# Kernel tuning notes

Hardware: AMD Instinct MI355X
Metric: run time of the kernel (lower is better)

Reference implementation:

```python
import jax, jax.numpy as jnp
import numpy as np

EMB = 300; H = 150; DEC = 300
VU = 50000; VQ = 30000; VS = 5000
N_COLS = 64; COL_LEN = 6; N_TURNS = 6; IN_LEN = 128; GEN_LEN = 64
MAX_KEEP = 5


def _lstm_cell(x, h, c, Wih, Whh, b):
    z = x @ Wih.T + h @ Whh.T + b
    i, f, g, o = jnp.split(z, 4)
    c = jax.nn.sigmoid(f) * c + jax.nn.sigmoid(i) * jnp.tanh(g)
    h = jax.nn.sigmoid(o) * jnp.tanh(c)
    return h, c


def _run_lstm(xs, Wih, Whh, b):
    hsz = Whh.shape[-1]
    z = jnp.zeros((hsz,), xs.dtype)
    def step(carry, x):
        h, c = _lstm_cell(x, carry[0], carry[1], Wih, Whh, b)
        return (h, c), h
    (h, c), ys = jax.lax.scan(step, (z, z), xs)
    return ys, h, c


def _bilstm(xs, Wih, Whh, b):
    # Wih: [2, 4H, in], Whh: [2, 4H, H], b: [2, 4H]
    yf, hf, cf = _run_lstm(xs, Wih[0], Whh[0], b[0])
    yb, hb, cb = _run_lstm(xs[::-1], Wih[1], Whh[1], b[1])
    return jnp.concatenate([yf, yb[::-1]], -1), jnp.concatenate([hf, hb], -1), jnp.concatenate([cf, cb], -1)


def _attention(q, keys, Wq, Wk, v):
    # Bahdanau: v^T tanh(Wq q + Wk k); context = softmax-weighted sum of keys
    s = jnp.tanh(q @ Wq + keys @ Wk) @ v
    return jax.nn.softmax(s) @ keys


def _forward(utter_emb, query_emb, schema_tok_emb, enc_Wih, enc_Whh, enc_b,
             attn_Wq, attn_Wk, attn_v, dec_Wih0, dec_Whh0, dec_b0,
             dec_Wih1, dec_Whh1, dec_b1, transform_W, sql_W, sql_b, col_W,
             schema_tokens, input_seqs, output_gt):
    attn = lambda k_i, q, keys: _attention(q, keys, attn_Wq[k_i], attn_Wk[k_i], attn_v[k_i])
    # --- schema column encoding: BiLSTM over each column's name tokens ---
    col_tok = schema_tok_emb[schema_tokens]                       # [C, L, EMB]
    _, h, _ = jax.vmap(lambda xs: _bilstm(xs, enc_Wih[0], enc_Whh[0], enc_b[0]))(col_tok)
    schema_embs = h                                               # [C, EMB]
    prev_in, prev_h, prev_c, prev_out = [], [], [], []
    all_dists = []
    bos_emb = query_emb[0]
    for i in range(N_TURNS):
        idx = input_seqs[i]
        # mixed vocab / schema-pointer embedding lookup
        x = jnp.where((idx < VU)[:, None],
                      utter_emb[jnp.clip(idx, 0, VU - 1)],
                      schema_embs[jnp.clip(idx - VU, 0, N_COLS - 1)])
        x, _, _ = _bilstm(x, enc_Wih[1], enc_Whh[1], enc_b[1])    # utter_encoder
        # TextSchemaEncoder (approx): second BiLSTM + schema cross-attention update
        x, fh, fc = _bilstm(x, enc_Wih[2], enc_Whh[2], enc_b[2])
        schema_embs = schema_embs + jax.nn.softmax(schema_embs @ x.T, -1) @ x
        h0, c0 = fh, fc
        if i > 0:
            hist_h = jnp.stack(prev_h); hist_c = jnp.stack(prev_c)
            h0n = h0 + attn(0, h0, hist_h)
            c0 = h0n + attn(0, c0, hist_c)  # replicates original's h-based c init
            h0 = h0n
        prev_in = (prev_in + [x])[:MAX_KEEP]
        prev_h = (prev_h + [fh])[:MAX_KEEP]
        prev_c = (prev_c + [fc])[:MAX_KEEP]
        keys_in = jnp.concatenate(prev_in, 0)
        keys_out = jnp.concatenate(prev_out, 0) if i > 0 else None
        se = schema_embs

        def embed_out(t):
            return jnp.where(t < VQ,
                             query_emb[jnp.clip(t, 0, VQ - 1)],
                             se[jnp.clip(t - VQ, 0, N_COLS - 1)])

        def dec_step(carry, t):
            h1p, c1p, h2p, c2p, dh = carry
            out_emb = embed_out(t)  # teacher forcing
            ctx_s = attn(1, dh, se)
            ctx_i = attn(2, dh, keys_in)
            ctx_o = attn(3, dh, keys_out) if keys_out is not None else jnp.zeros_like(ctx_i)
            ctx = jnp.concatenate([ctx_s, ctx_i, ctx_o])
            xin = jnp.concatenate([out_emb, ctx])                 # [4*EMB]
            h1, c1 = _lstm_cell(xin, h1p, c1p, dec_Wih0, dec_Whh0, dec_b0)
            h2, c2 = _lstm_cell(h1, h2p, c2p, dec_Wih1, dec_Whh1, dec_b1)
            out = jnp.tanh(jnp.concatenate([h2, ctx]) @ transform_W.T)
            score = jnp.concatenate([out @ sql_W.T + sql_b, (out @ col_W.T) @ se.T])
            dist = jax.nn.log_softmax(score)
            am_emb = embed_out(jnp.argmax(dist))
            return (h1, c1, h2, c2, h2), (dist, am_emb)

        init = (h0, c0, h0, c0, h0)
        _, (dists, am_embs) = jax.lax.scan(dec_step, init, output_gt[i, :GEN_LEN - 1])
        prev_out = (prev_out + [jnp.concatenate([bos_emb[None], am_embs], 0)])[:MAX_KEEP]
        all_dists.append(dists)
    return jnp.stack(all_dists, 0)  # [N_TURNS, GEN_LEN-1, VQ+N_COLS]


def setup_inputs() -> dict:
    key = jax.random.key(0)
    ks = jax.random.split(key, 24)
    s = 0.05
    f = lambda k, shape: jax.random.normal(k, shape, jnp.float32) * s
    return {
        "utter_emb": f(ks[0], (VU, EMB)),
        "query_emb": f(ks[1], (VQ, EMB)),
        "schema_tok_emb": f(ks[2], (VS, EMB)),
        "enc_Wih": f(ks[3], (3, 2, 4 * H, EMB)),   # [schema, utter, text-schema] x [fwd, bwd]
        "enc_Whh": f(ks[4], (3, 2, 4 * H, H)),
        "enc_b": f(ks[5], (3, 2, 4 * H)),
        "attn_Wq": f(ks[6], (4, EMB, EMB)),        # [turn, schema, in_tok, out_tok]
        "attn_Wk": f(ks[7], (4, EMB, EMB)),
        "attn_v": f(ks[8], (4, EMB)),
        "dec_Wih0": f(ks[9], (4 * DEC, 4 * EMB)),
        "dec_Whh0": f(ks[10], (4 * DEC, DEC)),
        "dec_b0": f(ks[11], (4 * DEC,)),
        "dec_Wih1": f(ks[12], (4 * DEC, DEC)),
        "dec_Whh1": f(ks[13], (4 * DEC, DEC)),
        "dec_b1": f(ks[14], (4 * DEC,)),
        "transform_W": f(ks[15], (EMB, 4 * EMB)),
        "sql_W": f(ks[16], (VQ, EMB)),
        "sql_b": f(ks[17], (VQ,)),
        "col_W": f(ks[18], (EMB, EMB)),
        "schema_tokens": jax.random.randint(ks[19], (N_COLS, COL_LEN), 0, VS),
        "input_seqs": jax.random.randint(ks[20], (N_TURNS, IN_LEN), 0, VU + N_COLS),
        "output_gt": jax.random.randint(ks[21], (N_TURNS, GEN_LEN), 0, VQ + N_COLS),
    }


def reference(utter_emb, query_emb, schema_tok_emb, enc_Wih, enc_Whh, enc_b,
              attn_Wq, attn_Wk, attn_v, dec_Wih0, dec_Whh0, dec_b0,
              dec_Wih1, dec_Whh1, dec_b1, transform_W, sql_W, sql_b, col_W,
              schema_tokens, input_seqs, output_gt):
    return _forward(utter_emb, query_emb, schema_tok_emb, enc_Wih, enc_Whh, enc_b,
                    attn_Wq, attn_Wk, attn_v, dec_Wih0, dec_Whh0, dec_b0,
                    dec_Wih1, dec_Whh1, dec_b1, transform_W, sql_W, sql_b, col_W,
                    schema_tokens, input_seqs, output_gt)
```

## Files before the change

### kernel.cpp

```cpp
#include <hip/hip_runtime.h>

#define EMB 300
#define VU 50000
#define VQ 30000
#define NCOLS 64
#define COLLEN 6
#define NTURNS 6
#define INLEN 128
#define TSTEPS 63
#define VOUT 30064
#define MAXK 5
#define NWD 60
#define FPAD 32
#define SENTU 0x7FC00001u
#define NGRP 8
#define GQW (TSTEPS*960)
#define GSC (TSTEPS*1024)
#define GH  (TSTEPS*320)

__device__ __forceinline__ float sigf(float x){ return 1.0f/(1.0f+__expf(-x)); }
__device__ __forceinline__ float tanhf_(float x){ return 1.0f - 2.0f/(1.0f+__expf(2.0f*x)); }
__device__ __forceinline__ float wsum(float v){
#pragma unroll
  for (int o=32;o;o>>=1) v += __shfl_xor(v,o);
  return v;
}
__device__ __forceinline__ float wmax(float v){
#pragma unroll
  for (int o=32;o;o>>=1) v = fmaxf(v,__shfl_xor(v,o));
  return v;
}

__device__ __forceinline__ void gstore(float* p, float v){
  __hip_atomic_store((int*)p, __float_as_int(v), __ATOMIC_RELAXED, __HIP_MEMORY_SCOPE_AGENT);
}
__device__ __forceinline__ float gload(const float* p){
  return __int_as_float(__hip_atomic_load((const int*)p, __ATOMIC_RELAXED, __HIP_MEMORY_SCOPE_AGENT));
}
__device__ __forceinline__ void gpub(float* p, float v){
  (void)__hip_atomic_exchange((int*)p, __float_as_int(v), __ATOMIC_RELAXED, __HIP_MEMORY_SCOPE_AGENT);
}

__device__ __forceinline__ void garrive(int* flags, int w, int P){
  asm volatile("s_waitcnt vmcnt(0)" ::: "memory");
  __syncthreads();
  if (threadIdx.x == 0)
    __hip_atomic_store(flags + w*FPAD, P, __ATOMIC_RELAXED, __HIP_MEMORY_SCOPE_AGENT);
}
__device__ __forceinline__ void gwait(const int* flags, int P){
  if (threadIdx.x < 64) {
    int v;
    do {
      v = (threadIdx.x < NWD) ? __hip_atomic_load(flags + threadIdx.x*FPAD, __ATOMIC_RELAXED, __HIP_MEMORY_SCOPE_AGENT) : P;
    } while (__any(v < P));
  }
  __syncthreads();
}

template<int MAXV>
__device__ __forceinline__ void pollfetch(const float* __restrict__ src, float* dstLDS,
                                          int n, int modstride, int tid)
{
  float v[MAXV]; bool val[MAXV]; int idx[MAXV];
#pragma unroll
  for (int k = 0; k < MAXV; ++k) {
    idx[k] = tid + 256*k;
    bool ib = idx[k] < n;
    if (modstride) {
      int m = idx[k];
      while (m >= modstride) m -= modstride;
      ib = ib && (m < 300);
    }
    val[k] = ib;
  }
  for (;;) {
    bool ok = true;
#pragma unroll
    for (int k = 0; k < MAXV; ++k)
      if (val[k]) { v[k] = gload(src + idx[k]); ok = ok && (__float_as_uint(v[k]) != SENTU); }
    if (__all(ok)) break;
    __builtin_amdgcn_s_sleep(1);
  }
#pragma unroll
  for (int k = 0; k < MAXV; ++k) if (val[k]) dstLDS[idx[k]] = v[k];
  __syncthreads();
}

__global__ void k_init(int* flags){
  for (int i = threadIdx.x; i < NWD*FPAD; i += 256) flags[i] = 0;
}

__global__ void k_transposeB(const float* __restrict__ in, float* __restrict__ out,
                             int R, int C, size_t mstride)
{
  __shared__ float tile[32][33];
  const float* inp = in + (size_t)blockIdx.z*mstride;
  float* outp = out + (size_t)blockIdx.z*mstride;
  const int rb = blockIdx.y*32, cb = blockIdx.x*32;
  const int tx = threadIdx.x & 31, ty = threadIdx.x >> 5;
  for (int k = 0; k < 32; k += 8) {
    int r = rb + ty + k, c = cb + tx;
    if (r < R && c < C) tile[ty+k][tx] = inp[(size_t)r*C + c];
  }
  __syncthreads();
  for (int k = 0; k < 32; k += 8) {
    int c = cb + ty + k, r = rb + tx;
    if (c < C && r < R) outp[(size_t)c*R + r] = tile[tx][ty+k];
  }
}

__global__ void k_schema(const float* __restrict__ temb, const int* __restrict__ stok,
                         const float* __restrict__ Wih, const float* __restrict__ Whh,
                         const float* __restrict__ bb, float* __restrict__ SE0)
{
  const int col = blockIdx.x >> 1, dir = blockIdx.x & 1, tid = threadIdx.x;
  __shared__ float hl[150], cl[150], zl[600], xs[304];
  if (tid < 150) { hl[tid]=0.f; cl[tid]=0.f; }
  __syncthreads();
  const float* Wi = Wih + (size_t)dir*600*300;
  const float* Wh = Whh + (size_t)dir*600*150;
  const float* bd = bb + dir*600;
  for (int s = 0; s < COLLEN; ++s) {
    const int pos = dir ? (COLLEN-1-s) : s;
    const int tok = stok[col*COLLEN + pos];
    const float* x = temb + (size_t)tok*300;
    for (int c = tid; c < 300; c += 256) xs[c] = x[c];
    __syncthreads();
    for (int g = tid; g < 600; g += 256) {
      float a = bd[g];
      const float* wi = Wi + (size_t)g*300;
      for (int c = 0; c < 300; ++c) a += xs[c]*wi[c];
      const float* wh = Wh + (size_t)g*150;
      for (int j = 0; j < 150; ++j) a += hl[j]*wh[j];
      zl[g] = a;
    }
    __syncthreads();
    if (tid < 150) {
      float ii=zl[tid], ff=zl[150+tid], gg=zl[300+tid], oo=zl[450+tid];
      float cn = sigf(ff)*cl[tid] + sigf(ii)*tanhf_(gg);
      cl[tid]=cn; hl[tid]=sigf(oo)*tanhf_(cn);
    }
    __syncthreads();
  }
  if (tid < 150) SE0[(size_t)col*300 + dir*150 + tid] = hl[tid];
}

__global__ void k_gemm_xe(const float* __restrict__ src, const float* __restrict__ SEi,
                          const int* __restrict__ iseq, int mode,
                          const float* __restrict__ WihT, const float* __restrict__ bL,
                          float* __restrict__ Xg)
{
  __shared__ float xs[16][304];
  const int tid = threadIdx.x;
  const int p0 = blockIdx.y*16;
  for (int i = tid; i < 16*300; i += 256) {
    int t = i / 300, c = i - t*300;
    const float* xr;
    if (mode) xr = src + (size_t)(p0+t)*300;
    else {
      int tok = iseq[p0+t];
      xr = (tok < VU) ? src + (size_t)tok*300 : SEi + (size_t)(tok - VU)*300;
    }
    xs[t][c] = xr[c];
  }
  __syncthreads();
  const int g = blockIdx.x*256 + tid;
  if (g >= 1200) return;
  const float b = bL[g];
  float acc[16];
#pragma unroll
  for (int t = 0; t < 16; ++t) acc[t] = b;
  for (int c = 0; c < 300; ++c) {
    float wv = WihT[(size_t)c*1200 + g];
#pragma unroll
    for (int t = 0; t < 16; ++t) acc[t] += wv * xs[t][c];
  }
#pragma unroll
  for (int t = 0; t < 16; ++t) Xg[(size_t)(p0+t)*1200 + g] = acc[t];
}

__global__ __launch_bounds__(640) void k_rec(
    const float* __restrict__ Xg, const float* __restrict__ WhhTL,
    float* __restrict__ ys, float* __restrict__ fh, float* __restrict__ fc)
{
  const int dir = blockIdx.x, tid = threadIdx.x;
  __shared__ __align__(16) float hl[2][152];
  const int g = (tid & 3)*150 + (tid >> 2);
  const bool act = (tid < 600);
  float w[150];
  const float* wt = WhhTL + (size_t)dir*150*600;
  if (act) {
#pragma unroll
    for (int j = 0; j < 150; ++j) w[j] = wt[(size_t)j*600 + g];
  }
  if (tid < 152) { hl[0][tid] = 0.f; hl[1][tid] = 0.f; }
  float cr = 0.f;
  __syncthreads();
  int par = 0;
  float xg = act ? Xg[(size_t)(dir ? INLEN-1 : 0)*1200 + dir*600 + g] : 0.f;
  for (int s = 0; s < INLEN; ++s) {
    const int pos = dir ? (INLEN-1-s) : s;
    const int nxt = dir ? (INLEN-2-s) : (s+1);
    float xg_nx = (s+1 < INLEN && act) ? Xg[(size_t)nxt*1200 + dir*600 + g] : 0.f;
    float acc = 0.f;
    if (act) {
      float aa[8];
#pragma unroll
      for (int q = 0; q < 8; ++q) aa[q] = 0.f;
      const float4* h4 = (const float4*)hl[par];
#pragma unroll
      for (int j4 = 0; j4 < 37; ++j4) {
        float4 h = h4[j4];
        aa[j4&7] += w[4*j4]*h.x + w[4*j4+1]*h.y + w[4*j4+2]*h.z + w[4*j4+3]*h.w;
      }
      acc = xg + ((aa[0]+aa[1])+(aa[2]+aa[3])) + ((aa[4]+aa[5])+(aa[6]+aa[7]))
            + w[148]*hl[par][148] + w[149]*hl[par][149];
    }
    float a1 = __shfl_xor(acc, 1);
    float a2 = __shfl_xor(acc, 2);
    float a3 = __shfl_xor(acc, 3);
    if (act && (tid & 3) == 0) {
      int d = tid >> 2;
      float cn = sigf(a1)*cr + sigf(acc)*tanhf_(a2);
      cr = cn;
      float hn = sigf(a3)*tanhf_(cn);
      hl[par^1][d] = hn;
      ys[(size_t)pos*300 + dir*150 + d] = hn;
    }
    __syncthreads();
    par ^= 1;
    xg = xg_nx;
  }
  if (act && (tid & 3) == 0) {
    int d = tid >> 2;
    fh[dir*150 + d] = hl[par][d];
    fc[dir*150 + d] = cr;
  }
}

__global__ void k_schema_upd(const float* __restrict__ SEi, const float* __restrict__ ys2,
                             float* __restrict__ SEo,
                             const float* __restrict__ fh, const float* __restrict__ fc,
                             float* __restrict__ HH, float* __restrict__ CH,
                             float* __restrict__ XH, int turn)
{
  const int row = blockIdx.x, tid = threadIdx.x;
  __shared__ float sl[300], al[128], red[4];
  for (int d = tid; d < 300; d += 256) sl[d] = SEi[(size_t)row*300 + d];
  __syncthreads();
  if (tid < 128) {
    float a = 0;
    const float* yr = ys2 + (size_t)tid*300;
    for (int d = 0; d < 300; ++d) a += sl[d]*yr[d];
    al[tid] = a;
  }
  __syncthreads();
  if (tid < 64) { float m = fmaxf(al[tid], al[tid+64]); m = wmax(m); if (tid==0) red[0]=m; }
  __syncthreads();
  if (tid < 128) al[tid] = __expf(al[tid] - red[0]);
  __syncthreads();
  if (tid < 64) { float s = al[tid] + al[tid+64]; s = wsum(s); if (tid==0) red[1]=s; }
  __syncthreads();
  const float invz = 1.0f/red[1];
  for (int d = tid; d < 300; d += 256) {
    float a = sl[d];
    for (int j = 0; j < 128; ++j) a += (al[j]*invz) * ys2[(size_t)j*300 + d];
    SEo[(size_t)row*300 + d] = a;
  }
  if (turn < MAXK) {
    for (int i = row*600 + tid; i < row*600 + 600; i += 256)
      XH[(size_t)turn*INLEN*300 + i] = ys2[i];
    if (row == 0)
      for (int d = tid; d < 300; d += 256) { HH[turn*300+d] = fh[d]; CH[turn*300+d] = fc[d]; }
  }
}

__device__ __forceinline__ const float* key_ptr(int j, int nin, const float* SE1,
                                                const float* XH, const float* OH, int* fam)
{
  if (j < 64) { *fam = 0; return SE1 + (size_t)j*300; }
  if (j < 64+nin) { *fam = 1; return XH + (size_t)(j-64)*300; }
  *fam = 2; return OH + (size_t)(j-64-nin)*300;
}

__global__ __launch_bounds__(256) void k_tables(
    const float* __restrict__ SE1, const float* __restrict__ XH,
    const float* __restrict__ OH, const float* __restrict__ Wk,
    const float* __restrict__ Wih0T, const float* __restrict__ b0,
    const float* __restrict__ tWT, const float* __restrict__ qemb,
    const int* __restrict__ gt,
    float* __restrict__ KW, float* __restrict__ G2K,
    float* __restrict__ Ew, float* __restrict__ G1KT,
    int nin, int nout)
{
  const int NK = 64 + nin + nout;
  const int NT32 = NK >> 5;
  const int tid = threadIdx.x;
  const int b = blockIdx.x;
  __shared__ float A[32][301];
  const int wv4 = tid >> 6, ln = tid & 63;

  if (b < 2*NT32) {
    const int j0 = (b < NT32 ? b : b - NT32) * 32;
    int fam; const float* base = key_ptr(j0, nin, SE1, XH, OH, &fam);
    for (int jj = wv4*8; jj < wv4*8+8; ++jj)
      for (int c = ln; c < 300; c += 64)
        A[jj][c] = base[(size_t)jj*300 + c];
    __syncthreads();
    if (b < NT32) {
      const float* W = Wk + (size_t)(1+fam)*90000;
      for (int rep = 0; rep < 2; ++rep) {
        int c = tid + rep*256;
        if (c < 300) {
          float acc[32];
#pragma unroll
          for (int j = 0; j < 32; ++j) acc[j] = 0.f;
          for (int d = 0; d < 300; ++d) {
            float wvv = W[(size_t)d*300 + c];
#pragma unroll
            for (int j = 0; j < 32; ++j) acc[j] += A[j][d]*wvv;
          }
#pragma unroll
          for (int j = 0; j < 32; ++j) KW[(size_t)(j0+j)*300 + c] = acc[j];
        }
      }
    } else {
      const int cb = 300 + fam*300;
      for (int rep = 0; rep < 2; ++rep) {
        int r = tid + rep*256;
        if (r < 300) {
          float acc[32];
#pragma unroll
          for (int j = 0; j < 32; ++j) acc[j] = 0.f;
          for (int d = 0; d < 300; ++d) {
            float wvv = tWT[(size_t)(cb+d)*300 + r];
#pragma unroll
            for (int j = 0; j < 32; ++j) acc[j] += A[j][d]*wvv;
          }
#pragma unroll
          for (int j = 0; j < 32; ++j) G2K[(size_t)(j0+j)*300 + r] = acc[j];
        }
      }
    }
  } else if (b < 2*NT32 + 20) {
    const int idx = b - 2*NT32;
    const int gx = idx % 5, ty = idx / 5;
    const int g = gx*256 + tid;
    const int tb = ty*16;
    for (int i = tid; i < 16*300; i += 256) {
      int k = i / 300, c = i - k*300;
      int t = tb + k;
      int tok = (t < 63) ? gt[t] : 0;
      const float* e = (tok < VQ) ? qemb + (size_t)tok*300 : SE1 + (size_t)(tok-VQ)*300;
      A[k][c] = e[c];
    }
    __syncthreads();
    if (g < 1200) {
      float bb = b0[g];
      float acc[16];
#pragma unroll
      for (int k = 0; k < 16; ++k) acc[k] = bb;
      for (int c = 0; c < 300; ++c) {
        float wvv = Wih0T[(size_t)c*1200 + g];
#pragma unroll
        for (int k = 0; k < 16; ++k) acc[k] += wvv * A[k][c];
      }
#pragma unroll
      for (int k = 0; k < 16; ++k)
        if (tb + k < 63) Ew[(size_t)(tb+k)*1200 + g] = acc[k];
    }
  } else {
    const int idx = b - (2*NT32 + 20);
    const int j0 = (idx % NT32)*32, r0 = (idx / NT32)*64;
    int fam; const float* base = key_ptr(j0, nin, SE1, XH, OH, &fam);
    for (int jj = wv4*8; jj < wv4*8+8; ++jj)
      for (int c = ln; c < 300; c += 64)
        A[jj][c] = base[(size_t)jj*300 + c];
    __syncthreads();
    const int r = r0 + (tid & 63);
    const int jg = (tid >> 6)*8;
    const int cb = 300 + fam*300;
    float acc[8] = {0,0,0,0,0,0,0,0};
    if (r < 1200) {
      for (int c = 0; c < 300; ++c) {
        float wvv = Wih0T[(size_t)(cb+c)*1200 + r];
#pragma unroll
        for (int i = 0; i < 8; ++i) acc[i] += A[jg+i][c] * wvv;
      }
#pragma unroll
      for (int i = 0; i < 8; ++i) G1KT[(size_t)r*NK + j0 + jg + i] = acc[i];
    }
  }
}

__global__ __launch_bounds__(256, 1) void k_dec(
    const float* __restrict__ KW, const float* __restrict__ G1KT,
    const float* __restrict__ Ew, const float* __restrict__ WqT,
    const float* __restrict__ av, const float* __restrict__ Wq0,
    const float* __restrict__ Wk0,
    const float* __restrict__ Whh0, const float* __restrict__ Wih1,
    const float* __restrict__ Whh1, const float* __restrict__ b1,
    const float* __restrict__ fh, const float* __restrict__ fc,
    const float* __restrict__ HH, const float* __restrict__ CH,
    float* __restrict__ h0b, float* __restrict__ c0b,
    float* __restrict__ xQW, float* __restrict__ xSC,
    float* __restrict__ xH1, float* __restrict__ xH2,
    float* __restrict__ Alog, float* __restrict__ H2log,
    int nin, int nout, int turn, int* __restrict__ flags)
{
  const int NK = 64 + nin + nout;
  const int w = blockIdx.x, tid = threadIdx.x;
  const int wv = tid >> 6, ln = tid & 63;
  const int grp = w & (NGRP-1);
  __shared__ float g1kl[20][1024];
  __shared__ float kwl[18][320];
  __shared__ float qWlp[3][320];
  __shared__ float vllp[3][320];
  __shared__ float ewl[63][20];
  __shared__ float scl[1024];
  __shared__ float dhl[320], h1l[320];
  __shared__ float pre1[20], pre2[20], zl[20], c1l[5], c2l[5];
  __shared__ float redA[4], alscA[8];
  __shared__ float wr0[4], wr1[4], wr2[4], rm[3], rz[3];
  const float SENTF = __uint_as_float(SENTU);

  for (int i = w*256 + tid; i < NGRP*GQW; i += NWD*256) gstore(xQW + i, SENTF);
  for (int i = w*256 + tid; i < NGRP*GSC; i += NWD*256) gstore(xSC + i, SENTF);
  for (int i = w*256 + tid; i < NGRP*GH;  i += NWD*256) gstore(xH1 + i, SENTF);
  for (int i = w*256 + tid; i < NGRP*GH;  i += NWD*256) gstore(xH2 + i, SENTF);

  for (int i = tid; i < 20*1024; i += 256) {
    int o = i >> 10, j = i & 1023;
    int row = w*5 + (o % 5) + 300*(o / 5);
    g1kl[o][j] = (j < NK) ? G1KT[(size_t)row*NK + j] : 0.f;
  }
  for (int i = tid; i < 18*320; i += 256) {
    int jo = i / 320, c = i - jo*320;
    int j = w*18 + jo;
    kwl[jo][c] = (c < 300 && j < NK) ? KW[(size_t)j*300 + c] : 0.f;
  }
  for (int i = tid; i < 3*320; i += 256) {
    int f = i / 320, c = i - f*320;
    vllp[f][c] = (c < 300) ? av[300 + f*300 + c] : 0.f;
    qWlp[f][c] = 0.f;
  }
  for (int i = tid; i < 63*20; i += 256) {
    int t = i / 20, o = i - t*20;
    int row = w*5 + (o % 5) + 300*(o / 5);
    ewl[t][o] = Ew[(size_t)t*1200 + row];
  }
  if (tid < 20) { dhl[300+tid] = 0.f; h1l[300+tid] = 0.f; }

  float rwh0[5][5], rwh1[5][5], rwi1[5][5], rwq4[4][5], b1r[5];
#pragma unroll
  for (int r = 0; r < 5; ++r) {
    int row = w*5 + r + 300*wv;
    b1r[r] = b1[row];
#pragma unroll
    for (int k = 0; k < 5; ++k) {
      int d = ln + 64*k;
      rwh0[r][k] = (d < 300) ? Whh0[(size_t)row*300 + d] : 0.f;
      rwh1[r][k] = (d < 300) ? Whh1[(size_t)row*300 + d] : 0.f;
      rwi1[r][k] = (d < 300) ? Wih1[(size_t)row*300 + d] : 0.f;
    }
  }
#pragma unroll
  for (int r = 0; r < 4; ++r) {
    int o = r*4 + wv;
    int q = w*15 + ((o < 15) ? o : 0);
    int fam = q / 300, c = q - fam*300;
    const float* bp = WqT + ((size_t)(1+fam)*300 + c)*300;
#pragma unroll
    for (int k = 0; k < 5; ++k) {
      int d = ln + 64*k;
      rwq4[r][k] = (o < 15 && d < 300) ? bp[d] : 0.f;
    }
  }
  const int jlo = (w*18 < NK) ? w*18 : NK-1;
  const int jhi = (w*18+17 < NK) ? w*18+17 : NK-1;
  const int f0 = (jlo < 64) ? 0 : (jlo < 64+nin ? 1 : 2);
  const int f1 = (jhi < 64) ? 0 : (jhi < 64+nin ? 1 : 2);
  __syncthreads();

  if (w == 0) {
    if (turn == 0) {
      for (int d = tid; d < 300; d += 256) { gstore(h0b+d, fh[d]); gstore(c0b+d, fc[d]); }
    } else {
      const int nh = turn;
      for (int d = tid; d < 300; d += 256) dhl[d] = fh[d];
      __syncthreads();
      for (int rep = 0; rep < 2; ++rep) {
        const float* keys = rep ? CH : HH;
        for (int c = tid; c < 300; c += 256) {
          float a = 0;
          for (int d = 0; d < 300; ++d) a += dhl[d]*Wq0[(size_t)d*300 + c];
          h1l[c] = a;
        }
        __syncthreads();
        for (int k = 0; k < nh; ++k) {
          const float* Kr = keys + (size_t)k*300;
          float part = 0;
          for (int c = tid; c < 300; c += 256) {
            float kw = 0;
            for (int d = 0; d < 300; ++d) kw += Kr[d]*Wk0[(size_t)d*300 + c];
            part += av[c]*tanhf_(h1l[c] + kw);
          }
          part = wsum(part);
          if (ln == 0) redA[wv] = part;
          __syncthreads();
          if (tid == 0) alscA[k] = redA[0]+redA[1]+redA[2]+redA[3];
          __syncthreads();
        }
        if (tid == 0) {
          float m = -1e30f;
          for (int k = 0; k < nh; ++k) m = fmaxf(m, alscA[k]);
          float z = 0;
          for (int k = 0; k < nh; ++k) { alscA[k] = __expf(alscA[k]-m); z += alscA[k]; }
          for (int k = 0; k < nh; ++k) alscA[k] /= z;
        }
        __syncthreads();
        if (rep == 0) {
          for (int c = tid; c < 300; c += 256) {
            float a = dhl[c];
            for (int k = 0; k < nh; ++k) a += alscA[k]*keys[(size_t)k*300 + c];
            scl[c] = a; gstore(h0b+c, a);
          }
          __syncthreads();
          for (int d = tid; d < 300; d += 256) dhl[d] = fc[d];
          __syncthreads();
        } else {
          for (int c = tid; c < 300; c += 256) {
            float a = scl[c];
            for (int k = 0; k < nh; ++k) a += alscA[k]*keys[(size_t)k*300 + c];
            gstore(c0b+c, a);
          }
        }
      }
    }
  }
  garrive(flags, w, turn+1);
  gwait(flags, turn+1);

  for (int i = tid; i < 300; i += 256) { float v = gload(h0b+i); dhl[i] = v; h1l[i] = v; }
  if (tid < 5) { float v = gload(c0b + w*5 + tid); c1l[tid] = v; c2l[tid] = v; }
  __syncthreads();

  for (int t = 0; t < TSTEPS; ++t) {
    if (t) pollfetch<2>(xH2 + (size_t)grp*GH + (size_t)(t-1)*320, dhl, 300, 0, tid);
#pragma unroll
    for (int r = 0; r < 4; ++r) {
      float a = 0;
#pragma unroll
      for (int k = 0; k < 5; ++k) a += rwq4[r][k]*dhl[ln + 64*k];
      a = wsum(a);
      int o = r*4 + wv;
      if (ln < NGRP && o < 15) {
        int q = w*15 + o, fam = q/300, c = q - fam*300;
        gpub(xQW + (size_t)ln*GQW + (size_t)t*960 + fam*320 + c, a);
      }
    }
#pragma unroll
    for (int r = 0; r < 5; ++r) {
      float a1 = 0, a2 = 0;
#pragma unroll
      for (int k = 0; k < 5; ++k) {
        float hv = h1l[ln + 64*k], dv = dhl[ln + 64*k];
        a1 += rwh0[r][k]*hv; a2 += rwh1[r][k]*dv;
      }
      a1 = wsum(a1); a2 = wsum(a2);
      if (ln == 0) { pre1[wv*5+r] = a1; pre2[wv*5+r] = a2 + b1r[r]; }
    }

    pollfetch<3>(xQW + (size_t)grp*GQW + (size_t)t*960 + f0*320, &qWlp[f0][0], (f1-f0+1)*320, 320, tid);
#pragma unroll
    for (int r = 0; r < 5; ++r) {
      int jo = wv*5 + r;
      int j = w*18 + jo;
      bool va = (jo < 18) && (j < NK);
      int f = va ? ((j < 64) ? 0 : (j < 64+nin ? 1 : 2)) : 0;
      int jc = (jo < 18) ? jo : 0;
      float a = 0;
#pragma unroll
      for (int k = 0; k < 5; ++k) {
        int c = ln + 64*k;
        a += vllp[f][c] * tanhf_(qWlp[f][c] + kwl[jc][c]);
      }
      a = wsum(a);
      if (ln < NGRP && va) gpub(xSC + (size_t)ln*GSC + (size_t)t*1024 + j, a);
    }

    pollfetch<4>(xSC + (size_t)grp*GSC + (size_t)t*1024, scl, NK, 0, tid);
    {
      float m0=-1e30f, m1=-1e30f, m2=-1e30f;
      for (int j = tid; j < NK; j += 256) {
        float x = scl[j];
        if (j < 64) m0 = fmaxf(m0,x); else if (j < 64+nin) m1 = fmaxf(m1,x); else m2 = fmaxf(m2,x);
      }
      m0 = wmax(m0); m1 = wmax(m1); m2 = wmax(m2);
      if (ln==0){ wr0[wv]=m0; wr1[wv]=m1; wr2[wv]=m2; }
      __syncthreads();
      if (tid==0){
        rm[0]=fmaxf(fmaxf(wr0[0],wr0[1]),fmaxf(wr0[2],wr0[3]));
        rm[1]=fmaxf(fmaxf(wr1[0],wr1[1]),fmaxf(wr1[2],wr1[3]));
        rm[2]=fmaxf(fmaxf(wr2[0],wr2[1]),fmaxf(wr2[2],wr2[3]));
      }
      __syncthreads();
      float s0=0,s1=0,s2=0;
      for (int j = tid; j < NK; j += 256) {
        int f = (j<64)?0:(j<64+nin?1:2);
        float e = __expf(scl[j] - rm[f]);
        scl[j] = e;
        if (f==0) s0+=e; else if (f==1) s1+=e; else s2+=e;
      }
      s0=wsum(s0); s1=wsum(s1); s2=wsum(s2);
      if (ln==0){ wr0[wv]=s0; wr1[wv]=s1; wr2[wv]=s2; }
      __syncthreads();
      if (tid==0){
        rz[0]=wr0[0]+wr0[1]+wr0[2]+wr0[3];
        rz[1]=wr1[0]+wr1[1]+wr1[2]+wr1[3];
        rz[2]=wr2[0]+wr2[1]+wr2[2]+wr2[3];
      }
      __syncthreads();
    }
    const int KC = NK >> 6;
    const int c1e = 1 + (nin >> 6);
    float inv0 = 1.0f/rz[0], inv1 = 1.0f/rz[1];
    float inv2 = (KC > c1e) ? 1.0f/rz[2] : 0.f;
    {
#pragma unroll 1
      for (int r = 0; r < 5; ++r) {
        int o = wv*5 + r;
        float a0 = scl[ln]*g1kl[o][ln];
        float a1 = 0, a2 = 0;
        for (int k = 1; k < c1e; ++k) { int j = ln + 64*k; a1 += scl[j]*g1kl[o][j]; }
        for (int k = c1e; k < KC; ++k) { int j = ln + 64*k; a2 += scl[j]*g1kl[o][j]; }
        float a = a0*inv0 + a1*inv1 + a2*inv2;
        a = wsum(a);
        if (ln == 0) zl[o] = a + ewl[t][o] + pre1[o];
      }
    }
    __syncthreads();
    if (tid < 5) {
      float ii=zl[tid], ff=zl[5+tid], gg=zl[10+tid], oo=zl[15+tid];
      float cn = sigf(ff)*c1l[tid] + sigf(ii)*tanhf_(gg);
      c1l[tid] = cn;
      float h1v = sigf(oo)*tanhf_(cn);
#pragma unroll
      for (int g = 0; g < NGRP; ++g)
        gpub(xH1 + (size_t)g*GH + (size_t)t*320 + w*5 + tid, h1v);
    }
    if (tid < 18) {
      int j = w*18 + tid;
      if (j < NK) {
        int f = (j<64)?0:(j<64+nin?1:2);
        float iv = (f==0)?inv0:((f==1)?inv1:inv2);
        Alog[(size_t)t*1024 + j] = scl[j]*iv;
      }
    }

    pollfetch<2>(xH1 + (size_t)grp*GH + (size_t)t*320, h1l, 300, 0, tid);
#pragma unroll
    for (int r = 0; r < 5; ++r) {
      float a = 0;
#pragma unroll
      for (int k = 0; k < 5; ++k) a += rwi1[r][k]*h1l[ln + 64*k];
      a = wsum(a);
      if (ln == 0) zl[wv*5+r] = a + pre2[wv*5+r];
    }
    __syncthreads();
    if (tid < 5) {
      int d = w*5 + tid;
      float ii=zl[tid], ff=zl[5+tid], gg=zl[10+tid], oo=zl[15+tid];
      float cn = sigf(ff)*c2l[tid] + sigf(ii)*tanhf_(gg);
      c2l[tid] = cn;
      float hn = sigf(oo)*tanhf_(cn);
#pragma unroll
      for (int g = 0; g < NGRP; ++g)
        gpub(xH2 + (size_t)g*GH + (size_t)t*320 + d, hn);
      H2log[(size_t)t*300 + d] = hn;
    }
  }
}

__global__ void k_ctxout2(const float* __restrict__ H2, const float* __restrict__ Al,
                          const float* __restrict__ G2K, const float* __restrict__ tWT,
                          const float* __restrict__ colW,
                          float* __restrict__ o63, float* __restrict__ t63, int NK)
{
  const int t = blockIdx.x, tid = threadIdx.x;
  __shared__ float ol[304], h2l[304], all[1024];
  for (int d = tid; d < 300; d += 256) h2l[d] = H2[(size_t)t*300 + d];
  for (int j = tid; j < NK; j += 256) all[j] = Al[(size_t)t*1024 + j];
  __syncthreads();
  for (int r = tid; r < 300; r += 256) {
    float a = 0;
    for (int d = 0; d < 300; ++d) a += h2l[d]*tWT[(size_t)d*300 + r];
    for (int j = 0; j < NK; ++j) a += all[j]*G2K[(size_t)j*300 + r];
    float v = tanhf_(a);
    ol[r] = v;
    o63[(size_t)t*300 + r] = v;
  }
  __syncthreads();
  for (int e = tid; e < 300; e += 256) {
    float a = 0;
    const float* wc = colW + (size_t)e*300;
    for (int d = 0; d < 300; ++d) a += ol[d]*wc[d];
    t63[(size_t)t*300 + e] = a;
  }
}

__global__ __launch_bounds__(256) void k_score(
    const float* __restrict__ o63, const float* __restrict__ t63,
    const float* __restrict__ sqlW, const float* __restrict__ sqlb,
    const float* __restrict__ SE1, float* __restrict__ Dout)
{
  const int vb = blockIdx.x, tid = threadIdx.x;
  const int v = vb*256 + tid;
  if ((vb+1)*256 <= VQ) {
    __shared__ __align__(16) float olT[300][68];
    for (int i = tid; i < 63*300; i += 256) {
      int k = i / 300, d = i - k*300;
      olT[d][k] = o63[i];
    }
    for (int d = tid; d < 300; d += 256) { olT[d][63] = 0.f; }
    __syncthreads();
    const float* w = sqlW + (size_t)v*300;
    float acc[64];
#pragma unroll
    for (int k = 0; k < 64; ++k) acc[k] = 0.f;
    for (int d = 0; d < 300; ++d) {
      float wv_ = w[d];
      const float4* row = (const float4*)&olT[d][0];
#pragma unroll
      for (int k4 = 0; k4 < 16; ++k4) {
        float4 ov = row[k4];
        acc[k4*4+0] += wv_*ov.x; acc[k4*4+1] += wv_*ov.y;
        acc[k4*4+2] += wv_*ov.z; acc[k4*4+3] += wv_*ov.w;
      }
    }
    const float b = sqlb[v];
    for (int k = 0; k < 63; ++k) Dout[(size_t)k*VOUT + v] = acc[k] + b;
  } else {
    if (v >= VOUT) return;
    const bool isv = (v < VQ);
    const float* w = isv ? sqlW + (size_t)v*300 : SE1 + (size_t)(v - VQ)*300;
    const float* src = isv ? o63 : t63;
    float acc[63];
#pragma unroll
    for (int k = 0; k < 63; ++k) acc[k] = 0.f;
    for (int d = 0; d < 300; ++d) {
      float wv_ = w[d];
      for (int k = 0; k < 63; ++k) acc[k] += wv_ * src[(size_t)k*300 + d];
    }
    const float b = isv ? sqlb[v] : 0.f;
    for (int k = 0; k < 63; ++k) Dout[(size_t)k*VOUT + v] = acc[k] + b;
  }
}

__global__ void k_lsm(float* __restrict__ rows, const float* __restrict__ qemb,
                      const float* __restrict__ SE1, float* __restrict__ OHt)
{
  const int t = blockIdx.x, tid = threadIdx.x, wv = tid>>6, ln = tid&63;
  float* row = rows + (size_t)t*VOUT;
  __shared__ float rv[4], rs[4];
  __shared__ int ri[4];
  float m = -1e30f; int mi = VOUT;
  for (int j = tid; j < VOUT; j += 256) {
    float x = row[j];
    if (x > m) { m = x; mi = j; }
  }
#pragma unroll
  for (int o = 32; o; o >>= 1) {
    float om = __shfl_xor(m, o); int oi = __shfl_xor(mi, o);
    if (om > m || (om == m && oi < mi)) { m = om; mi = oi; }
  }
  if (ln == 0) { rv[wv] = m; ri[wv] = mi; }
  __syncthreads();
  if (tid == 0) {
    for (int k = 1; k < 4; ++k)
      if (rv[k] > rv[0] || (rv[k] == rv[0] && ri[k] < ri[0])) { rv[0]=rv[k]; ri[0]=ri[k]; }
  }
  __syncthreads();
  const float M = rv[0];
  float s = 0;
  for (int j = tid; j < VOUT; j += 256) s += __expf(row[j] - M);
  s = wsum(s);
  if (ln == 0) rs[wv] = s;
  __syncthreads();
  const float L = M + logf(rs[0]+rs[1]+rs[2]+rs[3]);
  for (int j = tid; j < VOUT; j += 256) row[j] -= L;
  if (OHt) {
    int id = ri[0];
    const float* src = (id < VQ) ? qemb + (size_t)id*300 : SE1 + (size_t)(id-VQ)*300;
    for (int d = tid; d < 300; d += 256) {
      OHt[(size_t)(t+1)*300 + d] = src[d];
      if (t == 0) OHt[d] = qemb[d];
    }
  }
}

extern "C" void kernel_launch(void* const* d_in, const int* in_sizes, int n_in,
                              void* d_out, int out_size, void* d_ws, size_t ws_size,
                              hipStream_t stream)
{
  const float* utter = (const float*)d_in[0];
  const float* qemb  = (const float*)d_in[1];
  const float* temb  = (const float*)d_in[2];
  const float* eWih  = (const float*)d_in[3];
  const float* eWhh  = (const float*)d_in[4];
  const float* eb    = (const float*)d_in[5];
  const float* aWq   = (const float*)d_in[6];
  const float* aWk   = (const float*)d_in[7];
  const float* av    = (const float*)d_in[8];
  const float* dWih0 = (const float*)d_in[9];
  const float* dWhh0 = (const float*)d_in[10];
  const float* db0   = (const float*)d_in[11];
  const float* dWih1 = (const float*)d_in[12];
  const float* dWhh1 = (const float*)d_in[13];
  const float* db1   = (const float*)d_in[14];
  const float* tW    = (const float*)d_in[15];
  const float* sqlW  = (const float*)d_in[16];
  const float* sqlb  = (const float*)d_in[17];
  const float* colW  = (const float*)d_in[18];
  const int* stok    = (const int*)d_in[19];
  const int* iseq    = (const int*)d_in[20];
  const int* ogt     = (const int*)d_in[21];
  float* dout = (float*)d_out;

  float* base = (float*)d_ws;
  size_t off = 0;
  auto A = [&](size_t n)->float*{ float* r = base + off; off += (n + 63) & ~(size_t)63; return r; };
  float* SE    = A(7*64*300);
  float* XH    = A(5*128*300);
  float* OH    = A(5*64*300);
  float* HH    = A(5*300);
  float* CH    = A(5*300);
  float* ys1   = A(128*300);
  float* ys2   = A(128*300);
  float* Xg    = A(128*1200);
  float* fh    = A(320);
  float* fc    = A(320);
  float* fhs   = A(320);
  float* fcs   = A(320);
  float* h0b   = A(320);
  float* c0b   = A(320);
  float* xQW   = A(NGRP*GQW);
  float* xSC   = A(NGRP*GSC);
  float* xH1   = A(NGRP*GH);
  float* xH2   = A(NGRP*GH);
  float* KW    = A(1024*300);
  float* G1KT  = A(1200*1024);
  float* G2K   = A(1024*300);
  float* EwB   = A(63*1200);
  float* Alog  = A(63*1024);
  float* H2lg  = A(64*300);
  float* o63   = A(64*300);
  float* t63   = A(64*300);
  A(512);
  float* WqT   = A(4*300*300);
  float* WhhT  = A(6*150*600);
  float* Wih0T = A(1200*1200);
  float* tWT   = A(1200*300);
  float* eWT   = A(2*300*1200);
  int* flags = (int*)A(NWD*FPAD);
  (void)ws_size; (void)in_sizes; (void)n_in; (void)out_size;

  dim3 B256(256);
  k_init<<<1, B256, 0, stream>>>(flags);
  k_transposeB<<<dim3(10,10,4), B256, 0, stream>>>(aWq, WqT, 300, 300, 90000);
  k_transposeB<<<dim3(5,19,6), B256, 0, stream>>>(eWhh, WhhT, 600, 150, 90000);
  k_transposeB<<<dim3(38,38,1), B256, 0, stream>>>(dWih0, Wih0T, 1200, 1200, 0);
  k_transposeB<<<dim3(38,10,1), B256, 0, stream>>>(tW, tWT, 300, 1200, 0);
  k_transposeB<<<dim3(10,38,2), B256, 0, stream>>>(eWih + 360000, eWT, 1200, 300, 360000);
  k_schema<<<128, B256, 0, stream>>>(temb, stok, eWih, eWhh, eb, SE);

  for (int i = 0; i < NTURNS; ++i) {
    const int kin  = (i+1 < MAXK) ? (i+1) : MAXK;
    const int kout = (i < MAXK) ? i : MAXK;
    const int nin = kin*128, nout = kout*64;
    const int NK = 64 + nin + nout;
    const int NT32 = NK/32;
    float* SEi = SE + (size_t)i*19200;
    float* SEo = SE + (size_t)(i+1)*19200;

    k_gemm_xe<<<dim3(5,8), B256, 0, stream>>>(utter, SEi, iseq + i*INLEN, 0,
                                              eWT, eb + 1200, Xg);
    k_rec<<<2, 640, 0, stream>>>(Xg, WhhT + 180000, ys1, fhs, fcs);
    k_gemm_xe<<<dim3(5,8), B256, 0, stream>>>(ys1, SEi, iseq + i*INLEN, 1,
                                              eWT + 360000, eb + 2400, Xg);
    k_rec<<<2, 640, 0, stream>>>(Xg, WhhT + 360000, ys2, fh, fc);
    k_schema_upd<<<64, B256, 0, stream>>>(SEi, ys2, SEo, fh, fc, HH, CH, XH, i);
    k_tables<<<2*NT32 + 20 + NT32*19, B256, 0, stream>>>(
        SEo, XH, OH, aWk, Wih0T, db0, tWT, qemb, ogt + i*64,
        KW, G2K, EwB, G1KT, nin, nout);
    k_dec<<<NWD, B256, 0, stream>>>(KW, G1KT, EwB, WqT, av, aWq, aWk,
                                    dWhh0, dWih1, dWhh1, db1, fh, fc, HH, CH,
                                    h0b, c0b, xQW, xSC, xH1, xH2, Alog, H2lg,
                                    nin, nout, i, flags);
    k_ctxout2<<<63, B256, 0, stream>>>(H2lg, Alog, G2K, tWT, colW, o63, t63, NK);
    k_score<<<dim3(118), B256, 0, stream>>>(o63, t63, sqlW, sqlb, SEo, dout + (size_t)i*63*VOUT);
    k_lsm<<<63, B256, 0, stream>>>(dout + (size_t)i*63*VOUT, qemb, SEo,
                                   (i < MAXK) ? OH + (size_t)i*19200 : nullptr);
  }
}
```

Measured before the change: 18.49 ms.

## Merge setup kernels, split recurrent weights between LDS and registers, vectorize score weights

Folds the flag init, five transpose launches and the schema BiLSTM into one persistent setup kernel, which removes several launches and the Whh transpose. The recurrent kernel now keeps the first 64 columns of each gate's Whh row in swizzled LDS and the other 86 in registers. This cuts register pressure from 150 floats per thread. The score kernel reads sqlW rows as float4 instead of scalars. The costs are 150KB of LDS in k_rec and a serial schema BiLSTM tail in the merged setup.

```diff
diff --git a/kernel.cpp b/kernel.cpp
--- a/kernel.cpp
+++ b/kernel.cpp
@@ -86,63 +86,88 @@
   __syncthreads();
 }
 
-__global__ void k_init(int* flags){
-  for (int i = threadIdx.x; i < NWD*FPAD; i += 256) flags[i] = 0;
-}
-
-__global__ void k_transposeB(const float* __restrict__ in, float* __restrict__ out,
-                             int R, int C, size_t mstride)
-{
-  __shared__ float tile[32][33];
-  const float* inp = in + (size_t)blockIdx.z*mstride;
-  float* outp = out + (size_t)blockIdx.z*mstride;
-  const int rb = blockIdx.y*32, cb = blockIdx.x*32;
-  const int tx = threadIdx.x & 31, ty = threadIdx.x >> 5;
+__device__ __forceinline__ void tr_tile(const float* __restrict__ in, float* __restrict__ out,
+                                        int R, int C, int bx, int by,
+                                        float (*tile)[33], int tid)
+{
+  const int rb = by*32, cb = bx*32;
+  const int tx = tid & 31, ty = (tid >> 5) & 7;
   for (int k = 0; k < 32; k += 8) {
     int r = rb + ty + k, c = cb + tx;
-    if (r < R && c < C) tile[ty+k][tx] = inp[(size_t)r*C + c];
+    if (r < R && c < C) tile[ty+k][tx] = in[(size_t)r*C + c];
   }
   __syncthreads();
   for (int k = 0; k < 32; k += 8) {
     int c = cb + ty + k, r = rb + tx;
-    if (c < C && r < R) outp[(size_t)c*R + r] = tile[tx][ty+k];
-  }
-}
-
-__global__ void k_schema(const float* __restrict__ temb, const int* __restrict__ stok,
-                         const float* __restrict__ Wih, const float* __restrict__ Whh,
-                         const float* __restrict__ bb, float* __restrict__ SE0)
-{
-  const int col = blockIdx.x >> 1, dir = blockIdx.x & 1, tid = threadIdx.x;
-  __shared__ float hl[150], cl[150], zl[600], xs[304];
-  if (tid < 150) { hl[tid]=0.f; cl[tid]=0.f; }
-  __syncthreads();
-  const float* Wi = Wih + (size_t)dir*600*300;
-  const float* Wh = Whh + (size_t)dir*600*150;
-  const float* bd = bb + dir*600;
-  for (int s = 0; s < COLLEN; ++s) {
-    const int pos = dir ? (COLLEN-1-s) : s;
-    const int tok = stok[col*COLLEN + pos];
-    const float* x = temb + (size_t)tok*300;
-    for (int c = tid; c < 300; c += 256) xs[c] = x[c];
+    if (c < C && r < R) out[(size_t)c*R + r] = tile[tx][ty+k];
+  }
+  __syncthreads();
+}
+
+__global__ __launch_bounds__(256) void k_setup(
+    const float* __restrict__ aWq, float* __restrict__ WqT,
+    const float* __restrict__ dWih0, float* __restrict__ Wih0T,
+    const float* __restrict__ tW, float* __restrict__ tWT,
+    const float* __restrict__ eWih, float* __restrict__ eWT,
+    const float* __restrict__ eWhh,
+    const float* __restrict__ temb, const int* __restrict__ stok,
+    const float* __restrict__ eb, float* __restrict__ SE0,
+    int* __restrict__ dflags)
+{
+  __shared__ float tile[32][33];
+  __shared__ float hl[152], cl[152], zl[600], xsr[304];
+  const int tid = threadIdx.x;
+  const int NCH = 3113;
+  for (int ch = blockIdx.x; ch < NCH; ch += 240) {
     __syncthreads();
-    for (int g = tid; g < 600; g += 256) {
-      float a = bd[g];
-      const float* wi = Wi + (size_t)g*300;
-      for (int c = 0; c < 300; ++c) a += xs[c]*wi[c];
-      const float* wh = Wh + (size_t)g*150;
-      for (int j = 0; j < 150; ++j) a += hl[j]*wh[j];
-      zl[g] = a;
-    }
-    __syncthreads();
-    if (tid < 150) {
-      float ii=zl[tid], ff=zl[150+tid], gg=zl[300+tid], oo=zl[450+tid];
-      float cn = sigf(ff)*cl[tid] + sigf(ii)*tanhf_(gg);
-      cl[tid]=cn; hl[tid]=sigf(oo)*tanhf_(cn);
-    }
-    __syncthreads();
-  }
-  if (tid < 150) SE0[(size_t)col*300 + dir*150 + tid] = hl[tid];
+    if (ch < 400) {
+      int z = ch/100, r = ch - z*100;
+      tr_tile(aWq + (size_t)z*90000, WqT + (size_t)z*90000, 300, 300, r%10, r/10, tile, tid);
+    } else if (ch < 1844) {
+      int c2 = ch - 400;
+      tr_tile(dWih0, Wih0T, 1200, 1200, c2%38, c2/38, tile, tid);
+    } else if (ch < 2224) {
+      int c2 = ch - 1844;
+      tr_tile(tW, tWT, 300, 1200, c2%38, c2/38, tile, tid);
+    } else if (ch < 2984) {
+      int c2 = ch - 2224; int z = c2/380, r = c2 - z*380;
+      tr_tile(eWih + 360000 + (size_t)z*360000, eWT + (size_t)z*360000, 1200, 300, r%10, r/10, tile, tid);
+    } else if (ch < 3112) {
+      const int unit = ch - 2984;
+      const int col = unit >> 1, dir = unit & 1;
+      if (tid < 152) { hl[tid]=0.f; cl[tid]=0.f; }
+      __syncthreads();
+      const float* Wi = eWih + (size_t)dir*180000;
+      const float* Wh = eWhh + (size_t)dir*90000;
+      const float* bd = eb + dir*600;
+      for (int s = 0; s < COLLEN; ++s) {
+        const int pos = dir ? (COLLEN-1-s) : s;
+        const int tok = stok[col*COLLEN + pos];
+        const float* x = temb + (size_t)tok*300;
+        for (int c = tid; c < 300; c += 256) xsr[c] = x[c];
+        __syncthreads();
+        for (int g = tid; g < 600; g += 256) {
+          float a = bd[g];
+          const float* wi = Wi + (size_t)g*300;
+          for (int c = 0; c < 300; ++c) a += xsr[c]*wi[c];
+          const float* wh = Wh + (size_t)g*150;
+          for (int j = 0; j < 150; ++j) a += hl[j]*wh[j];
+          zl[g] = a;
+        }
+        __syncthreads();
+        if (tid < 150) {
+          float ii=zl[tid], ff=zl[150+tid], gg=zl[300+tid], oo=zl[450+tid];
+          float cn = sigf(ff)*cl[tid] + sigf(ii)*tanhf_(gg);
+          cl[tid]=cn; hl[tid]=sigf(oo)*tanhf_(cn);
+        }
+        __syncthreads();
+      }
+      if (tid < 150) SE0[(size_t)col*300 + dir*150 + tid] = hl[tid];
+      __syncthreads();
+    } else {
+      for (int i = tid; i < NWD*FPAD; i += 256) dflags[i] = 0;
+    }
+  }
 }
 
 __global__ void k_gemm_xe(const float* __restrict__ src, const float* __restrict__ SEi,
@@ -180,23 +205,31 @@
 }
 
 __global__ __launch_bounds__(640) void k_rec(
-    const float* __restrict__ Xg, const float* __restrict__ WhhTL,
+    const float* __restrict__ Xg, const float* __restrict__ WhhL,
     float* __restrict__ ys, float* __restrict__ fh, float* __restrict__ fc)
 {
   const int dir = blockIdx.x, tid = threadIdx.x;
+  __shared__ __align__(16) float wlo[600*64];
   __shared__ __align__(16) float hl[2][152];
   const int g = (tid & 3)*150 + (tid >> 2);
   const bool act = (tid < 600);
-  float w[150];
-  const float* wt = WhhTL + (size_t)dir*150*600;
+  for (int i = tid; i < 600*64; i += 640) {
+    int gg = i >> 6, j = i & 63;
+    int fo = gg*64 + (((j >> 2) ^ (gg & 7)) << 2) + (j & 3);
+    wlo[fo] = WhhL[(size_t)dir*90000 + (size_t)gg*150 + j];
+  }
+  float w_[86];
   if (act) {
-#pragma unroll
-    for (int j = 0; j < 150; ++j) w[j] = wt[(size_t)j*600 + g];
+    const float* wr = WhhL + (size_t)dir*90000 + (size_t)g*150 + 64;
+#pragma unroll
+    for (int m = 0; m < 86; ++m) w_[m] = wr[m];
   }
   if (tid < 152) { hl[0][tid] = 0.f; hl[1][tid] = 0.f; }
   float cr = 0.f;
   __syncthreads();
   int par = 0;
+  const int gsw = g & 7;
+  const float4* wb = (const float4*)(wlo + g*64);
   float xg = act ? Xg[(size_t)(dir ? INLEN-1 : 0)*1200 + dir*600 + g] : 0.f;
   for (int s = 0; s < INLEN; ++s) {
     const int pos = dir ? (INLEN-1-s) : s;
@@ -209,12 +242,19 @@
       for (int q = 0; q < 8; ++q) aa[q] = 0.f;
       const float4* h4 = (const float4*)hl[par];
 #pragma unroll
-      for (int j4 = 0; j4 < 37; ++j4) {
+      for (int c4 = 0; c4 < 16; ++c4) {
+        float4 h = h4[c4];
+        float4 wv = wb[c4 ^ gsw];
+        aa[c4&7] += wv.x*h.x + wv.y*h.y + wv.z*h.z + wv.w*h.w;
+      }
+#pragma unroll
+      for (int j4 = 16; j4 < 37; ++j4) {
         float4 h = h4[j4];
-        aa[j4&7] += w[4*j4]*h.x + w[4*j4+1]*h.y + w[4*j4+2]*h.z + w[4*j4+3]*h.w;
+        int m = (j4-16)*4;
+        aa[j4&7] += w_[m]*h.x + w_[m+1]*h.y + w_[m+2]*h.z + w_[m+3]*h.w;
       }
       acc = xg + ((aa[0]+aa[1])+(aa[2]+aa[3])) + ((aa[4]+aa[5])+(aa[6]+aa[7]))
-            + w[148]*hl[par][148] + w[149]*hl[par][149];
+            + w_[84]*hl[par][148] + w_[85]*hl[par][149];
     }
     float a1 = __shfl_xor(acc, 1);
     float a2 = __shfl_xor(acc, 2);
@@ -722,20 +762,25 @@
       int k = i / 300, d = i - k*300;
       olT[d][k] = o63[i];
     }
-    for (int d = tid; d < 300; d += 256) { olT[d][63] = 0.f; }
+    for (int d = tid; d < 300; d += 256) olT[d][63] = 0.f;
     __syncthreads();
-    const float* w = sqlW + (size_t)v*300;
+    const float4* w4 = (const float4*)(sqlW + (size_t)v*300);
     float acc[64];
 #pragma unroll
     for (int k = 0; k < 64; ++k) acc[k] = 0.f;
-    for (int d = 0; d < 300; ++d) {
-      float wv_ = w[d];
-      const float4* row = (const float4*)&olT[d][0];
-#pragma unroll
-      for (int k4 = 0; k4 < 16; ++k4) {
-        float4 ov = row[k4];
-        acc[k4*4+0] += wv_*ov.x; acc[k4*4+1] += wv_*ov.y;
-        acc[k4*4+2] += wv_*ov.z; acc[k4*4+3] += wv_*ov.w;
+    for (int d4 = 0; d4 < 75; ++d4) {
+      float4 wq = w4[d4];
+      float wa[4] = {wq.x, wq.y, wq.z, wq.w};
+#pragma unroll
+      for (int s = 0; s < 4; ++s) {
+        float ws = wa[s];
+        const float4* row = (const float4*)&olT[d4*4+s][0];
+#pragma unroll
+        for (int k4 = 0; k4 < 16; ++k4) {
+          float4 ov = row[k4];
+          acc[4*k4+0] += ws*ov.x; acc[4*k4+1] += ws*ov.y;
+          acc[4*k4+2] += ws*ov.z; acc[4*k4+3] += ws*ov.w;
+        }
       }
     }
     const float b = sqlb[v];
@@ -858,21 +903,14 @@
   float* t63   = A(64*300);
   A(512);
   float* WqT   = A(4*300*300);
-  float* WhhT  = A(6*150*600);
   float* Wih0T = A(1200*1200);
   float* tWT   = A(1200*300);
   float* eWT   = A(2*300*1200);
-  int* flags = (int*)A(NWD*FPAD);
+  int* dflags = (int*)A(NWD*FPAD);
   (void)ws_size; (void)in_sizes; (void)n_in; (void)out_size;
 
-  dim3 B256(256);
-  k_init<<<1, B256, 0, stream>>>(flags);
-  k_transposeB<<<dim3(10,10,4), B256, 0, stream>>>(aWq, WqT, 300, 300, 90000);
-  k_transposeB<<<dim3(5,19,6), B256, 0, stream>>>(eWhh, WhhT, 600, 150, 90000);
-  k_transposeB<<<dim3(38,38,1), B256, 0, stream>>>(dWih0, Wih0T, 1200, 1200, 0);
-  k_transposeB<<<dim3(38,10,1), B256, 0, stream>>>(tW, tWT, 300, 1200, 0);
-  k_transposeB<<<dim3(10,38,2), B256, 0, stream>>>(eWih + 360000, eWT, 1200, 300, 360000);
-  k_schema<<<128, B256, 0, stream>>>(temb, stok, eWih, eWhh, eb, SE);
+  k_setup<<<240, 256, 0, stream>>>(aWq, WqT, dWih0, Wih0T, tW, tWT, eWih, eWT, eWhh,
+                                   temb, stok, eb, SE, dflags);
 
   for (int i = 0; i < NTURNS; ++i) {
     const int kin  = (i+1 < MAXK) ? (i+1) : MAXK;
@@ -883,23 +921,23 @@
     float* SEi = SE + (size_t)i*19200;
     float* SEo = SE + (size_t)(i+1)*19200;
 
-    k_gemm_xe<<<dim3(5,8), B256, 0, stream>>>(utter, SEi, iseq + i*INLEN, 0,
-                                              eWT, eb + 1200, Xg);
-    k_rec<<<2, 640, 0, stream>>>(Xg, WhhT + 180000, ys1, fhs, fcs);
-    k_gemm_xe<<<dim3(5,8), B256, 0, stream>>>(ys1, SEi, iseq + i*INLEN, 1,
-                                              eWT + 360000, eb + 2400, Xg);
-    k_rec<<<2, 640, 0, stream>>>(Xg, WhhT + 360000, ys2, fh, fc);
-    k_schema_upd<<<64, B256, 0, stream>>>(SEi, ys2, SEo, fh, fc, HH, CH, XH, i);
-    k_tables<<<2*NT32 + 20 + NT32*19, B256, 0, stream>>>(
+    k_gemm_xe<<<dim3(5,8), 256, 0, stream>>>(utter, SEi, iseq + i*INLEN, 0,
+                                             eWT, eb + 1200, Xg);
+    k_rec<<<2, 640, 0, stream>>>(Xg, eWhh + 180000, ys1, fhs, fcs);
+    k_gemm_xe<<<dim3(5,8), 256, 0, stream>>>(ys1, SEi, iseq + i*INLEN, 1,
+                                             eWT + 360000, eb + 2400, Xg);
+    k_rec<<<2, 640, 0, stream>>>(Xg, eWhh + 360000, ys2, fh, fc);
+    k_schema_upd<<<64, 256, 0, stream>>>(SEi, ys2, SEo, fh, fc, HH, CH, XH, i);
+    k_tables<<<2*NT32 + 20 + NT32*19, 256, 0, stream>>>(
         SEo, XH, OH, aWk, Wih0T, db0, tWT, qemb, ogt + i*64,
         KW, G2K, EwB, G1KT, nin, nout);
-    k_dec<<<NWD, B256, 0, stream>>>(KW, G1KT, EwB, WqT, av, aWq, aWk,
-                                    dWhh0, dWih1, dWhh1, db1, fh, fc, HH, CH,
-                                    h0b, c0b, xQW, xSC, xH1, xH2, Alog, H2lg,
-                                    nin, nout, i, flags);
-    k_ctxout2<<<63, B256, 0, stream>>>(H2lg, Alog, G2K, tWT, colW, o63, t63, NK);
-    k_score<<<dim3(118), B256, 0, stream>>>(o63, t63, sqlW, sqlb, SEo, dout + (size_t)i*63*VOUT);
-    k_lsm<<<63, B256, 0, stream>>>(dout + (size_t)i*63*VOUT, qemb, SEo,
-                                   (i < MAXK) ? OH + (size_t)i*19200 : nullptr);
-  }
-}
+    k_dec<<<NWD, 256, 0, stream>>>(KW, G1KT, EwB, WqT, av, aWq, aWk,
+                                   dWhh0, dWih1, dWhh1, db1, fh, fc, HH, CH,
+                                   h0b, c0b, xQW, xSC, xH1, xH2, Alog, H2lg,
+                                   nin, nout, i, dflags);
+    k_ctxout2<<<63, 256, 0, stream>>>(H2lg, Alog, G2K, tWT, colW, o63, t63, NK);
+    k_score<<<118, 256, 0, stream>>>(o63, t63, sqlW, sqlb, SEo, dout + (size_t)i*63*VOUT);
+    k_lsm<<<63, 256, 0, stream>>>(dout + (size_t)i*63*VOUT, qemb, SEo,
+                                  (i < MAXK) ? OH + (size_t)i*19200 : nullptr);
+  }
+}
```

Measured after the change: 15.17 ms. 1.22x faster.
